# Kernel tuning notes

Measured on AMD Instinct MI355X. Metric: run time of the kernel, lower is better.

## Reference

```python
import jax, jax.numpy as jnp
import numpy as np

B, D, N, L, H, T = 256, 768, 256, 2, 8, 20
HD = D // H

def _ln(x, g, b):
    m = x.mean(-1, keepdims=True)
    v = ((x - m) ** 2).mean(-1, keepdims=True)
    return (x - m) / jnp.sqrt(v + 1e-5) * g + b

def setup_inputs() -> dict:
    key = jax.random.key(0)
    ks = jax.random.split(key, 8)
    kk = jax.random.split(ks[7], 10)
    def w(k, shape):
        return jax.random.normal(k, shape, jnp.float32) * 0.02
    return {
        'feats': jax.random.normal(ks[0], (B, D, N), jnp.float32),
        'past': jax.random.normal(ks[1], (B, 16, 6), jnp.float32),
        'w_qinit': w(ks[2], (121, D)), 'b_qinit': jnp.zeros((D,), jnp.float32),
        'pos_enc': w(ks[3], (1, N, D)),
        'w_pp': w(ks[4], (2, D)), 'b_pp': jnp.zeros((D,), jnp.float32),
        'g_pp': jnp.ones((D,), jnp.float32), 'be_pp': jnp.zeros((D,), jnp.float32),
        'time_emb': w(ks[5], (T, D)),
        'Wq': w(kk[0], (L, D, D)), 'bq': jnp.zeros((L, D), jnp.float32),
        'Wk': w(kk[1], (L, D, D)), 'bk': jnp.zeros((L, D), jnp.float32),
        'Wv': w(kk[2], (L, D, D)), 'bv': jnp.zeros((L, D), jnp.float32),
        'Wo': w(kk[3], (L, D, D)), 'bo': jnp.zeros((L, D), jnp.float32),
        'ln1_g': jnp.ones((L, D), jnp.float32), 'ln1_b': jnp.zeros((L, D), jnp.float32),
        'W1': w(kk[4], (L, D, 4 * D)), 'b1': jnp.zeros((L, 4 * D), jnp.float32),
        'W2': w(kk[5], (L, 4 * D, D)), 'b2': jnp.zeros((L, D), jnp.float32),
        'ln2_g': jnp.ones((L, D), jnp.float32), 'ln2_b': jnp.zeros((L, D), jnp.float32),
        'w_dec1': w(kk[6], (D, D)), 'b_dec1': jnp.zeros((D,), jnp.float32),
        'w_dec2': w(kk[7], (D, 2)), 'b_dec2': jnp.zeros((2,), jnp.float32),
        'intent': jax.random.randint(ks[6], (B,), 0, 3),
    }

def reference(feats, past, w_qinit, b_qinit, pos_enc, w_pp, b_pp, g_pp, be_pp,
              time_emb, Wq, bq, Wk, bk, Wv, bv, Wo, bo, ln1_g, ln1_b,
              W1, b1, W2, b2, ln2_g, ln2_b, w_dec1, b_dec1, w_dec2, b_dec2, intent):
    # tokens: [B, N, D]
    tokens = jnp.transpose(feats, (0, 2, 1)) + pos_enc
    onehot = jax.nn.one_hot(jnp.clip(intent - 1, 0, 2), 3, dtype=tokens.dtype)
    past_flat = past.reshape(B, -1)
    pad = jnp.zeros((B, 22), tokens.dtype)
    context = jnp.concatenate([onehot, past_flat, pad], axis=1) @ w_qinit + b_qinit  # [B, D]
    # precompute cross-attention K/V once per layer (tokens are constant across steps)
    Kh = (jnp.einsum('bnd,lde->lbne', tokens, Wk) + bk[:, None, None, :]).reshape(L, B, N, H, HD)
    Vh = (jnp.einsum('bnd,lde->lbne', tokens, Wv) + bv[:, None, None, :]).reshape(L, B, N, H, HD)
    scale = 1.0 / np.sqrt(HD)

    def step(carry, te):
        ctx, cp = carry
        pq = jax.nn.relu(_ln(cp @ w_pp + b_pp, g_pp, be_pp))
        x = (ctx + pq + te)[:, None, :]  # [B, 1, D]
        for l in range(L):
            q = (_ln(x, ln1_g[l], ln1_b[l]) @ Wq[l] + bq[l]).reshape(B, 1, H, HD)
            s = jnp.einsum('bqhd,bnhd->bhqn', q, Kh[l]) * scale
            a = jax.nn.softmax(s, axis=-1)
            o = jnp.einsum('bhqn,bnhd->bqhd', a, Vh[l]).reshape(B, 1, D) @ Wo[l] + bo[l]
            x = x + o
            h = jax.nn.gelu(_ln(x, ln2_g[l], ln2_b[l]) @ W1[l] + b1[l], approximate=False) @ W2[l] + b2[l]
            x = x + h
        ctx = x[:, 0]
        delta = jax.nn.gelu(ctx @ w_dec1 + b_dec1, approximate=False) @ w_dec2 + b_dec2
        cp = cp + delta
        return (ctx, cp), cp

    init = (context, past[:, -1, 0:2])
    _, ys = jax.lax.scan(step, init, time_emb)  # ys: [T, B, 2]
    return jnp.transpose(ys, (1, 0, 2))
```

## Files before the change

kernel.cpp:

```cpp
#include <hip/hip_runtime.h>
#include <hip/hip_bf16.h>
#include <math.h>

#define B_ 256
#define D_ 768
#define N_ 256
#define L_ 2
#define H_ 8
#define T_ 20
#define HD_ 96
#define D4_ 3072

typedef float f32x4v __attribute__((ext_vector_type(4)));
typedef __bf16 bf16x8v __attribute__((ext_vector_type(8)));

union V16 { uint4 u; bf16x8v v; };

__device__ __forceinline__ ushort f2b(float f) {
    union { float f; unsigned u; } x{f};
    unsigned r = x.u + 0x7fffu + ((x.u >> 16) & 1u);
    return (ushort)(r >> 16);
}
__device__ __forceinline__ float b2f(ushort s) {
    union { unsigned u; float f; } x{(unsigned)s << 16};
    return x.f;
}
__device__ __forceinline__ float gelu_f(float v) {
    return 0.5f * v * (1.0f + erff(v * 0.7071067811865476f));
}
__device__ __forceinline__ float dot8(const float* __restrict__ xp, uint4 u) {
    return xp[0] * b2f((ushort)(u.x & 0xffffu)) + xp[1] * b2f((ushort)(u.x >> 16))
         + xp[2] * b2f((ushort)(u.y & 0xffffu)) + xp[3] * b2f((ushort)(u.y >> 16))
         + xp[4] * b2f((ushort)(u.z & 0xffffu)) + xp[5] * b2f((ushort)(u.z >> 16))
         + xp[6] * b2f((ushort)(u.w & 0xffffu)) + xp[7] * b2f((ushort)(u.w >> 16));
}
__device__ __forceinline__ float blockSum(float v, float* red, int tid) {
    for (int off = 32; off; off >>= 1) v += __shfl_down(v, off, 64);
    int w = tid >> 6, lane = tid & 63;
    if (lane == 0) red[w] = v;
    __syncthreads();
    float r = red[0] + red[1] + red[2] + red[3];
    __syncthreads();
    return r;
}

__global__ __launch_bounds__(256) void context_kernel(const float* __restrict__ past,
                                                      const float* __restrict__ w_qinit,
                                                      const float* __restrict__ b_qinit,
                                                      const int* __restrict__ intent,
                                                      const float* __restrict__ w_pp,
                                                      const float* __restrict__ b_pp,
                                                      const float* __restrict__ g_pp,
                                                      const float* __restrict__ be_pp,
                                                      const float* __restrict__ te0,
                                                      float* __restrict__ x,
                                                      float* __restrict__ cp) {
    int b = blockIdx.x, tid = threadIdx.x;
    __shared__ float ps[96];
    __shared__ int oidx;
    __shared__ float red[4];
    if (tid < 96) ps[tid] = past[b * 96 + tid];
    if (tid == 0) {
        int iv = intent[b] - 1;
        oidx = iv < 0 ? 0 : (iv > 2 ? 2 : iv);
    }
    __syncthreads();
    float ctx[3];
    #pragma unroll
    for (int r = 0; r < 3; ++r) {
        int d = tid + r * 256;
        float acc = w_qinit[oidx * D_ + d] + b_qinit[d];
        #pragma unroll 8
        for (int p = 0; p < 96; ++p) acc += ps[p] * w_qinit[(3 + p) * D_ + d];
        ctx[r] = acc;
    }
    float c0 = ps[90], c1 = ps[91];
    if (tid == 0) { cp[b * 2] = c0; cp[b * 2 + 1] = c1; }
    float t[3];
    float s = 0, ss = 0;
    #pragma unroll
    for (int r = 0; r < 3; ++r) {
        int d = tid + r * 256;
        t[r] = c0 * w_pp[d] + c1 * w_pp[D_ + d] + b_pp[d];
        s += t[r]; ss += t[r] * t[r];
    }
    s = blockSum(s, red, tid);
    ss = blockSum(ss, red, tid);
    float mean = s * (1.0f / D_);
    float var = ss * (1.0f / D_) - mean * mean;
    float rinv = rsqrtf(var + 1e-5f);
    #pragma unroll
    for (int r = 0; r < 3; ++r) {
        int d = tid + r * 256;
        float pq = fmaxf((t[r] - mean) * rinv * g_pp[d] + be_pp[d], 0.0f);
        x[b * D_ + d] = ctx[r] + pq + te0[d];
    }
}

__global__ __launch_bounds__(256) void token_prep(const float* __restrict__ feats,
                                                  const float* __restrict__ pos_enc,
                                                  ushort* __restrict__ tokens) {
    int b = blockIdx.z;
    int d0 = blockIdx.x * 64, n0 = blockIdx.y * 64;
    __shared__ float tile[64][65];
    int tid = threadIdx.x;
    int nl = tid & 63, dl0 = tid >> 6;
    const float* fb = feats + ((size_t)b * D_ + d0) * N_ + n0;
    #pragma unroll
    for (int i = 0; i < 16; ++i) {
        int dl = dl0 + i * 4;
        tile[dl][nl] = fb[(size_t)dl * N_ + nl];
    }
    __syncthreads();
    int dq = (tid & 15) * 4;
    int ng = tid >> 4;
    #pragma unroll
    for (int i = 0; i < 4; ++i) {
        int nl2 = ng + i * 16;
        int n = n0 + nl2;
        float4 p = *(const float4*)(pos_enc + (size_t)n * D_ + d0 + dq);
        ushort4 o;
        o.x = f2b(tile[dq + 0][nl2] + p.x);
        o.y = f2b(tile[dq + 1][nl2] + p.y);
        o.z = f2b(tile[dq + 2][nl2] + p.z);
        o.w = f2b(tile[dq + 3][nl2] + p.w);
        *(ushort4*)&tokens[((size_t)b * N_ + n) * D_ + d0 + dq] = o;
    }
}

__global__ __launch_bounds__(256) void transpose_w(const float* __restrict__ W,
                                                   ushort* __restrict__ out,
                                                   const float* __restrict__ scale,
                                                   int K, int N) {
    __shared__ float t[32][33];
    int k0 = blockIdx.y * 32, n0 = blockIdx.x * 32;
    int tx = threadIdx.x & 31, ty = threadIdx.x >> 5;
    #pragma unroll
    for (int i = 0; i < 4; ++i)
        t[ty + i * 8][tx] = W[(size_t)(k0 + ty + i * 8) * N + n0 + tx];
    __syncthreads();
    #pragma unroll
    for (int i = 0; i < 4; ++i) {
        int n = n0 + ty + i * 8, k = k0 + tx;
        float v = t[tx][ty + i * 8];
        if (scale) v *= scale[k];
        out[(size_t)n * K + k] = f2b(v);
    }
}

__global__ __launch_bounds__(256) void bias_eff_kernel(const float* __restrict__ W,
                                                       const float* __restrict__ bias,
                                                       const float* __restrict__ lb,
                                                       float* __restrict__ be, int Nc) {
    int n = blockIdx.x * 256 + threadIdx.x;
    float a = bias[n];
    for (int k = 0; k < D_; ++k) a += lb[k] * W[(size_t)k * Nc + n];
    be[n] = a;
}

__global__ void kvbias_prep(const float* __restrict__ bk, const float* __restrict__ bv,
                            float* __restrict__ bc) {
    int i = blockIdx.x * 256 + threadIdx.x;
    int mi = i / D_, c = i % D_;
    int l = mi >> 1;
    bc[i] = (mi & 1 ? bv : bk)[l * D_ + c];
}

__global__ __launch_bounds__(256) void kv_gemm_mfma(const ushort* __restrict__ tokens,
                                                    const ushort* __restrict__ Wkvt,
                                                    const float* __restrict__ bias_kv,
                                                    ushort* __restrict__ Kt,
                                                    ushort* __restrict__ Vt) {
    int e0 = blockIdx.x * 128;
    int mi = e0 / D_;
    int ein = e0 % D_;
    int l = mi >> 1, isV = mi & 1;
    int m0 = blockIdx.y * 128;
    int b = m0 >> 8, ntok0 = m0 & 255;
    __shared__ ushort smem[17408];
    ushort* As = smem;
    ushort* Bs = smem + 128 * 40;
    int tid = threadIdx.x;
    int w = tid >> 6, lane = tid & 63, quad = lane >> 4, l16 = lane & 15;
    int wr = w >> 1, wc = w & 1;
    f32x4v acc[4][4];
    #pragma unroll
    for (int i = 0; i < 4; ++i)
        #pragma unroll
        for (int j = 0; j < 4; ++j) acc[i][j] = (f32x4v)(0.0f);

    for (int k0 = 0; k0 < D_; k0 += 32) {
        #pragma unroll
        for (int vv = 0; vv < 2; ++vv) {
            int v = tid + vv * 256;
            int row = v >> 2, kv = v & 3;
            *(uint4*)&As[row * 40 + kv * 8] =
                *(const uint4*)&tokens[(size_t)(m0 + row) * D_ + k0 + kv * 8];
            *(uint4*)&Bs[row * 40 + kv * 8] =
                *(const uint4*)&Wkvt[(size_t)(e0 + row) * D_ + k0 + kv * 8];
        }
        __syncthreads();
        V16 a[4], bb[4];
        #pragma unroll
        for (int i = 0; i < 4; ++i)
            a[i].u = *(const uint4*)&As[(wr * 64 + i * 16 + l16) * 40 + quad * 8];
        #pragma unroll
        for (int j = 0; j < 4; ++j)
            bb[j].u = *(const uint4*)&Bs[(wc * 64 + j * 16 + l16) * 40 + quad * 8];
        #pragma unroll
        for (int i = 0; i < 4; ++i)
            #pragma unroll
            for (int j = 0; j < 4; ++j)
                acc[i][j] = __builtin_amdgcn_mfma_f32_16x16x32_bf16(a[i].v, bb[j].v, acc[i][j], 0, 0, 0);
        __syncthreads();
    }

    float bcol[4];
    #pragma unroll
    for (int j = 0; j < 4; ++j)
        bcol[j] = bias_kv[e0 + wc * 64 + j * 16 + l16];

    ushort* Ct = smem;
    ushort* outbuf = isV ? Vt : Kt;
    #pragma unroll
    for (int i = 0; i < 4; ++i)
        #pragma unroll
        for (int j = 0; j < 4; ++j) {
            int e_l = wc * 64 + j * 16 + l16;
            int m_b = wr * 64 + i * 16 + quad * 4;
            ushort4 p;
            p.x = f2b(acc[i][j][0] + bcol[j]);
            p.y = f2b(acc[i][j][1] + bcol[j]);
            p.z = f2b(acc[i][j][2] + bcol[j]);
            p.w = f2b(acc[i][j][3] + bcol[j]);
            *(ushort4*)&Ct[e_l * 136 + m_b] = p;
        }
    __syncthreads();
    int e_l = tid >> 1, half = tid & 1;
    int c = ein + e_l;
    int h = c / HD_, hd = c % HD_;
    size_t dst = ((((size_t)l * B_ + b) * H_ + h) * HD_ + hd) * N_ + ntok0 + half * 64;
    #pragma unroll
    for (int p8 = 0; p8 < 8; ++p8)
        *(uint4*)&outbuf[dst + p8 * 8] = *(const uint4*)&Ct[e_l * 136 + half * 64 + p8 * 8];
}

template<int AVAR, int OMODE, int STATS, int KSPLIT>
__global__ __launch_bounds__(256) void gemm_s(const void* __restrict__ Av,
                                              const ushort* __restrict__ Bt,
                                              const float* __restrict__ bias,
                                              void* __restrict__ Cv,
                                              int K, int Nc) {
    __shared__ ushort As[64 * 40];
    __shared__ ushort Bs[64 * 40];
    __shared__ float smst[64][2];
    int tid = threadIdx.x;
    int m0 = blockIdx.y * 64, e0 = blockIdx.x * 64;
    int kslice = K / KSPLIT;
    int kbeg = blockIdx.z * kslice, kend = kbeg + kslice;
    int w = tid >> 6, lane = tid & 63, quad = lane >> 4, l16 = lane & 15;

    if (STATS) {
        int row = tid >> 2, part = tid & 3;
        const float* xr = (const float*)Av + (size_t)(m0 + row) * K + part * 192;
        float s = 0, ss = 0;
        #pragma unroll 4
        for (int i = 0; i < 192; i += 4) {
            float4 f = *(const float4*)(xr + i);
            s += f.x + f.y + f.z + f.w;
            ss += f.x * f.x + f.y * f.y + f.z * f.z + f.w * f.w;
        }
        s += __shfl_xor(s, 1, 64);  s += __shfl_xor(s, 2, 64);
        ss += __shfl_xor(ss, 1, 64); ss += __shfl_xor(ss, 2, 64);
        if (part == 0) {
            float mean = s * (1.0f / 768.0f);
            float var = ss * (1.0f / 768.0f) - mean * mean;
            smst[row][0] = mean;
            smst[row][1] = rsqrtf(var + 1e-5f);
        }
        __syncthreads();
    }

    bool doA = tid < 128;
    int t2 = tid & 127;
    f32x4v acc[4];
    #pragma unroll
    for (int i = 0; i < 4; ++i) acc[i] = (f32x4v)(0.0f);

    auto fetch = [&](int kk, int vv) -> uint4 {
        int v = t2 + vv * 128;
        int row = v >> 2, kq = v & 3;
        if (doA) {
            if (AVAR == 0) {
                return *(const uint4*)((const ushort*)Av + (size_t)(m0 + row) * K + kk + kq * 8);
            } else {
                const float* Af = (const float*)Av + (size_t)(m0 + row) * K + kk + kq * 8;
                float4 f0 = *(const float4*)Af;
                float4 f1 = *(const float4*)(Af + 4);
                float mn = smst[row][0], rs = smst[row][1];
                f0.x = (f0.x - mn) * rs; f0.y = (f0.y - mn) * rs;
                f0.z = (f0.z - mn) * rs; f0.w = (f0.w - mn) * rs;
                f1.x = (f1.x - mn) * rs; f1.y = (f1.y - mn) * rs;
                f1.z = (f1.z - mn) * rs; f1.w = (f1.w - mn) * rs;
                uint4 u;
                u.x = (unsigned)f2b(f0.x) | ((unsigned)f2b(f0.y) << 16);
                u.y = (unsigned)f2b(f0.z) | ((unsigned)f2b(f0.w) << 16);
                u.z = (unsigned)f2b(f1.x) | ((unsigned)f2b(f1.y) << 16);
                u.w = (unsigned)f2b(f1.z) | ((unsigned)f2b(f1.w) << 16);
                return u;
            }
        } else {
            return *(const uint4*)&Bt[(size_t)(e0 + row) * K + kk + kq * 8];
        }
    };
    auto stash = [&](int vv, uint4 u) {
        int v = t2 + vv * 128;
        int row = v >> 2, kq = v & 3;
        ushort* dst = doA ? As : Bs;
        *(uint4*)&dst[row * 40 + kq * 8] = u;
    };
    auto compute = [&]() {
        V16 bb;
        bb.u = *(const uint4*)&Bs[(w * 16 + l16) * 40 + quad * 8];
        #pragma unroll
        for (int i = 0; i < 4; ++i) {
            V16 a;
            a.u = *(const uint4*)&As[(i * 16 + l16) * 40 + quad * 8];
            acc[i] = __builtin_amdgcn_mfma_f32_16x16x32_bf16(a.v, bb.v, acc[i], 0, 0, 0);
        }
    };

    {
        uint4 p0 = fetch(kbeg, 0), p1 = fetch(kbeg, 1);
        stash(0, p0); stash(1, p1);
    }
    __syncthreads();
    for (int kk = kbeg + 32; kk < kend; kk += 32) {
        uint4 p0 = fetch(kk, 0), p1 = fetch(kk, 1);
        compute();
        __syncthreads();
        stash(0, p0); stash(1, p1);
        __syncthreads();
    }
    compute();

    int n = e0 + w * 16 + l16;
    float bn = 0.0f;
    if (OMODE != 2 || blockIdx.z == 0) bn = bias[n];
    #pragma unroll
    for (int i = 0; i < 4; ++i) {
        #pragma unroll
        for (int r = 0; r < 4; ++r) {
            int m = m0 + i * 16 + quad * 4 + r;
            float v = acc[i][r] + bn;
            if (OMODE == 1) v = gelu_f(v);
            if (OMODE == 2) atomicAdd((float*)Cv + (size_t)m * Nc + n, v);
            else            ((ushort*)Cv)[(size_t)m * Nc + n] = f2b(v);
        }
    }
}

__global__ __launch_bounds__(256) void attn_fused(const float* __restrict__ x,
                                                  const ushort* __restrict__ Wqt,
                                                  const float* __restrict__ bqe,
                                                  const ushort* __restrict__ Kt,
                                                  const ushort* __restrict__ Vt,
                                                  ushort* __restrict__ att) {
    int b = blockIdx.y, h = blockIdx.x, tid = threadIdx.x;
    __shared__ float xs[768];
    __shared__ float red[4];
    __shared__ float qs[96];
    __shared__ float spart[4][256];
    __shared__ float sc[256];
    __shared__ float opo[96];

    if (tid < 192) *(float4*)&xs[tid * 4] = *(const float4*)&x[(size_t)b * D_ + tid * 4];
    __syncthreads();

    float s = 0, ss = 0;
    #pragma unroll
    for (int r = 0; r < 3; ++r) { float v = xs[tid + r * 256]; s += v; ss += v * v; }
    s = blockSum(s, red, tid);
    ss = blockSum(ss, red, tid);
    float mean = s * (1.0f / D_);
    float var = ss * (1.0f / D_) - mean * mean;
    float rinv = rsqrtf(var + 1e-5f);
    #pragma unroll
    for (int r = 0; r < 3; ++r) { int d = tid + r * 256; xs[d] = (xs[d] - mean) * rinv; }
    __syncthreads();

    if (tid < 192) {
        int j = tid >> 1, kh = tid & 1;
        const ushort* wr = Wqt + (size_t)(h * HD_ + j) * D_ + kh * 384;
        const float* xp = xs + kh * 384;
        float acc = 0.0f;
        #pragma unroll 4
        for (int k = 0; k < 384; k += 8)
            acc += dot8(xp + k, *(const uint4*)&wr[k]);
        acc += __shfl_xor(acc, 1, 64);
        if (kh == 0) qs[j] = (acc + bqe[h * HD_ + j]) * 0.10206207261596575f;
    }
    __syncthreads();

    {
        int hq = tid >> 6, tg = tid & 63;
        const ushort* Kp = Kt + (size_t)(b * H_ + h) * HD_ * N_;
        float s0 = 0, s1 = 0, s2 = 0, s3 = 0;
        #pragma unroll 6
        for (int i = 0; i < 24; ++i) {
            int hd = hq * 24 + i;
            uint2 kk = *(const uint2*)&Kp[hd * N_ + tg * 4];
            float qv = qs[hd];
            s0 += qv * b2f((ushort)(kk.x & 0xffffu));
            s1 += qv * b2f((ushort)(kk.x >> 16));
            s2 += qv * b2f((ushort)(kk.y & 0xffffu));
            s3 += qv * b2f((ushort)(kk.y >> 16));
        }
        float4 sv4;
        sv4.x = s0; sv4.y = s1; sv4.z = s2; sv4.w = s3;
        *(float4*)&spart[hq][tg * 4] = sv4;
    }
    __syncthreads();

    float sv = spart[0][tid] + spart[1][tid] + spart[2][tid] + spart[3][tid];
    int w = tid >> 6, lane = tid & 63;
    float m = sv;
    for (int off = 32; off; off >>= 1) m = fmaxf(m, __shfl_xor(m, off, 64));
    if (lane == 0) red[w] = m;
    __syncthreads();
    m = fmaxf(fmaxf(red[0], red[1]), fmaxf(red[2], red[3]));
    __syncthreads();
    float e = expf(sv - m);
    float tot = blockSum(e, red, tid);
    sc[tid] = e / tot;
    __syncthreads();

    if (tid < 192) {
        int hd = tid >> 1, nh = tid & 1;
        const ushort* Vr = Vt + (size_t)(b * H_ + h) * HD_ * N_ + hd * N_ + nh * 128;
        const float* scp = sc + nh * 128;
        float o = 0.0f;
        #pragma unroll 4
        for (int i = 0; i < 16; ++i)
            o += dot8(scp + i * 8, *(const uint4*)&Vr[i * 8]);
        o += __shfl_xor(o, 1, 64);
        if (nh == 0) opo[hd] = o;
    }
    __syncthreads();
    if (tid < 96) att[(size_t)b * D_ + h * HD_ + tid] = f2b(opo[tid]);
}

__global__ __launch_bounds__(256) void tail_kernel(float* __restrict__ x,
                                                   const ushort* __restrict__ dec1t,
                                                   const float* __restrict__ b_dec1,
                                                   const float* __restrict__ w_dec2,
                                                   const float* __restrict__ b_dec2,
                                                   float* __restrict__ cp,
                                                   float* __restrict__ out,
                                                   const float* __restrict__ time_emb,
                                                   const float* __restrict__ w_pp,
                                                   const float* __restrict__ b_pp,
                                                   const float* __restrict__ g_pp,
                                                   const float* __restrict__ be_pp,
                                                   int t) {
    int b = blockIdx.x, tid = threadIdx.x;
    __shared__ float xs[768];
    __shared__ float red[4];
    #pragma unroll
    for (int r = 0; r < 3; ++r) xs[tid + r * 256] = x[b * D_ + tid + r * 256];
    __syncthreads();
    float d0 = 0, d1 = 0, d2 = 0;
    const ushort* w0 = dec1t + (size_t)tid * D_;
    const ushort* w1 = w0 + (size_t)256 * D_;
    const ushort* w2 = w0 + (size_t)512 * D_;
    #pragma unroll 2
    for (int k = 0; k < 768; k += 8) {
        d0 += dot8(xs + k, *(const uint4*)&w0[k]);
        d1 += dot8(xs + k, *(const uint4*)&w1[k]);
        d2 += dot8(xs + k, *(const uint4*)&w2[k]);
    }
    float v0 = gelu_f(d0 + b_dec1[tid]);
    float v1 = gelu_f(d1 + b_dec1[tid + 256]);
    float v2 = gelu_f(d2 + b_dec1[tid + 512]);
    float p0 = v0 * w_dec2[tid * 2]     + v1 * w_dec2[(tid + 256) * 2]     + v2 * w_dec2[(tid + 512) * 2];
    float p1 = v0 * w_dec2[tid * 2 + 1] + v1 * w_dec2[(tid + 256) * 2 + 1] + v2 * w_dec2[(tid + 512) * 2 + 1];
    p0 = blockSum(p0, red, tid);
    p1 = blockSum(p1, red, tid);
    float c0 = cp[b * 2] + p0 + b_dec2[0];
    float c1 = cp[b * 2 + 1] + p1 + b_dec2[1];
    if (tid == 0) {
        cp[b * 2] = c0;
        cp[b * 2 + 1] = c1;
        out[(b * T_ + t) * 2] = c0;
        out[(b * T_ + t) * 2 + 1] = c1;
    }
    if (t < T_ - 1) {
        const float* te = time_emb + (size_t)(t + 1) * D_;
        float tv[3];
        float s = 0, ss = 0;
        #pragma unroll
        for (int r = 0; r < 3; ++r) {
            int d = tid + r * 256;
            tv[r] = c0 * w_pp[d] + c1 * w_pp[D_ + d] + b_pp[d];
            s += tv[r]; ss += tv[r] * tv[r];
        }
        s = blockSum(s, red, tid);
        ss = blockSum(ss, red, tid);
        float mean = s * (1.0f / D_);
        float var = ss * (1.0f / D_) - mean * mean;
        float rinv = rsqrtf(var + 1e-5f);
        #pragma unroll
        for (int r = 0; r < 3; ++r) {
            int d = tid + r * 256;
            float pq = fmaxf((tv[r] - mean) * rinv * g_pp[d] + be_pp[d], 0.0f);
            x[b * D_ + d] += pq + te[d];
        }
    }
}

extern "C" void kernel_launch(void* const* d_in, const int* in_sizes, int n_in,
                              void* d_out, int out_size, void* d_ws, size_t ws_size,
                              hipStream_t stream) {
    const float* feats   = (const float*)d_in[0];
    const float* past    = (const float*)d_in[1];
    const float* w_qinit = (const float*)d_in[2];
    const float* b_qinit = (const float*)d_in[3];
    const float* pos_enc = (const float*)d_in[4];
    const float* w_pp    = (const float*)d_in[5];
    const float* b_pp    = (const float*)d_in[6];
    const float* g_pp    = (const float*)d_in[7];
    const float* be_pp   = (const float*)d_in[8];
    const float* time_emb= (const float*)d_in[9];
    const float* Wq      = (const float*)d_in[10];
    const float* bq      = (const float*)d_in[11];
    const float* Wk      = (const float*)d_in[12];
    const float* bk      = (const float*)d_in[13];
    const float* Wv      = (const float*)d_in[14];
    const float* bv      = (const float*)d_in[15];
    const float* Wo      = (const float*)d_in[16];
    const float* bo      = (const float*)d_in[17];
    const float* ln1_g   = (const float*)d_in[18];
    const float* ln1_b   = (const float*)d_in[19];
    const float* W1      = (const float*)d_in[20];
    const float* b1      = (const float*)d_in[21];
    const float* W2      = (const float*)d_in[22];
    const float* b2      = (const float*)d_in[23];
    const float* ln2_g   = (const float*)d_in[24];
    const float* ln2_b   = (const float*)d_in[25];
    const float* w_dec1  = (const float*)d_in[26];
    const float* b_dec1  = (const float*)d_in[27];
    const float* w_dec2  = (const float*)d_in[28];
    const float* b_dec2  = (const float*)d_in[29];
    const int*   intent  = (const int*)d_in[30];
    float* out = (float*)d_out;

    const size_t WD = (size_t)D_ * D_;
    const size_t WD4 = (size_t)D_ * D4_;
    const size_t kv_elems = (size_t)L_ * B_ * H_ * HD_ * N_;
    const size_t kv_l = (size_t)B_ * H_ * HD_ * N_;

    char* wp = (char*)d_ws;
    ushort* Kt     = (ushort*)wp; wp += kv_elems * 2;
    ushort* Vt     = (ushort*)wp; wp += kv_elems * 2;
    ushort* tokens = (ushort*)wp; wp += (size_t)B_ * N_ * D_ * 2;
    ushort* Wkvt   = (ushort*)wp; wp += 4 * WD * 2;
    ushort* Wqt    = (ushort*)wp; wp += 2 * WD * 2;
    ushort* Wot    = (ushort*)wp; wp += 2 * WD * 2;
    ushort* W1t    = (ushort*)wp; wp += 2 * WD4 * 2;
    ushort* W2t    = (ushort*)wp; wp += 2 * WD4 * 2;
    ushort* dec1t  = (ushort*)wp; wp += WD * 2;
    float* bias_kv = (float*)wp;  wp += 4 * D_ * 4;
    float* bqe     = (float*)wp;  wp += 2 * D_ * 4;
    float* b1e     = (float*)wp;  wp += 2 * D4_ * 4;
    float* x       = (float*)wp;  wp += (size_t)B_ * D_ * 4;
    ushort* attbuf = (ushort*)wp; wp += (size_t)B_ * D_ * 2;
    ushort* h1     = (ushort*)wp; wp += (size_t)B_ * D4_ * 2;
    float* cp      = (float*)wp;  wp += (size_t)B_ * 2 * 4;

    context_kernel<<<B_, 256, 0, stream>>>(past, w_qinit, b_qinit, intent,
                                           w_pp, b_pp, g_pp, be_pp, time_emb, x, cp);
    token_prep<<<dim3(12, 4, 256), 256, 0, stream>>>(feats, pos_enc, tokens);
    kvbias_prep<<<12, 256, 0, stream>>>(bk, bv, bias_kv);
    for (int l = 0; l < L_; ++l) {
        transpose_w<<<dim3(24, 24), 256, 0, stream>>>(Wk + l * WD, Wkvt + (2 * l + 0) * WD, nullptr, D_, D_);
        transpose_w<<<dim3(24, 24), 256, 0, stream>>>(Wv + l * WD, Wkvt + (2 * l + 1) * WD, nullptr, D_, D_);
        transpose_w<<<dim3(24, 24), 256, 0, stream>>>(Wq + l * WD, Wqt + l * WD, ln1_g + l * D_, D_, D_);
        transpose_w<<<dim3(24, 24), 256, 0, stream>>>(Wo + l * WD, Wot + l * WD, nullptr, D_, D_);
        transpose_w<<<dim3(96, 24), 256, 0, stream>>>(W1 + l * WD4, W1t + l * WD4, ln2_g + l * D_, D_, D4_);
        transpose_w<<<dim3(24, 96), 256, 0, stream>>>(W2 + l * WD4, W2t + l * WD4, nullptr, D4_, D_);
        bias_eff_kernel<<<3, 256, 0, stream>>>(Wq + l * WD, bq + l * D_, ln1_b + l * D_, bqe + l * D_, D_);
        bias_eff_kernel<<<12, 256, 0, stream>>>(W1 + l * WD4, b1 + l * D4_, ln2_b + l * D_, b1e + l * D4_, D4_);
    }
    transpose_w<<<dim3(24, 24), 256, 0, stream>>>(w_dec1, dec1t, nullptr, D_, D_);

    kv_gemm_mfma<<<dim3(24, 512), 256, 0, stream>>>(tokens, Wkvt, bias_kv, Kt, Vt);

    for (int t = 0; t < T_; ++t) {
        for (int l = 0; l < L_; ++l) {
            attn_fused<<<dim3(H_, B_), 256, 0, stream>>>(x, Wqt + l * WD, bqe + l * D_,
                                                         Kt + l * kv_l, Vt + l * kv_l, attbuf);
            gemm_s<0, 2, 0, 4><<<dim3(12, 4, 4), 256, 0, stream>>>(attbuf, Wot + l * WD,
                                                                   bo + l * D_, x, D_, D_);
            gemm_s<1, 1, 1, 1><<<dim3(48, 4), 256, 0, stream>>>(x, W1t + l * WD4,
                                                                b1e + l * D4_, h1, D_, D4_);
            gemm_s<0, 2, 0, 4><<<dim3(12, 4, 4), 256, 0, stream>>>(h1, W2t + l * WD4,
                                                                   b2 + l * D_, x, D4_, D_);
        }
        tail_kernel<<<B_, 256, 0, stream>>>(x, dec1t, b_dec1, w_dec2, b_dec2, cp, out,
                                            time_emb, w_pp, b_pp, g_pp, be_pp, t);
    }
}
```

Measured before the change: 7.202 ms.

## Double-buffer GEMM tiles via direct global-to-LDS loads and widen attention K reads

The KV projection GEMM and the generic gemm_s kernel now stage their tiles with global_load_lds straight into double-buffered shared memory, so the next K-slice loads while MFMAs run on the current one. This removes the register round trip and one barrier per iteration. The padded row stride of 40 becomes an unpadded 32, which may add LDS bank conflicts on the MFMA operand reads. Attention score computation now reads K with 16-byte loads and combines half-waves with a shuffle.

Measured after the change: 6.781 ms. -5.8%, faster.

```diff
diff --git a/kernel.cpp b/kernel.cpp
--- a/kernel.cpp
+++ b/kernel.cpp
@@ -42,6 +42,11 @@
     float r = red[0] + red[1] + red[2] + red[3];
     __syncthreads();
     return r;
+}
+__device__ __forceinline__ void gl_lds16(const ushort* g, ushort* l) {
+    __builtin_amdgcn_global_load_lds((const __attribute__((address_space(1))) unsigned int*)g,
+                                     (__attribute__((address_space(3))) unsigned int*)l,
+                                     16, 0, 0);
 }
 
 __global__ __launch_bounds__(256) void context_kernel(const float* __restrict__ past,
@@ -177,9 +182,7 @@
     int l = mi >> 1, isV = mi & 1;
     int m0 = blockIdx.y * 128;
     int b = m0 >> 8, ntok0 = m0 & 255;
-    __shared__ ushort smem[17408];
-    ushort* As = smem;
-    ushort* Bs = smem + 128 * 40;
+    __shared__ __align__(16) ushort smem[17408];
     int tid = threadIdx.x;
     int w = tid >> 6, lane = tid & 63, quad = lane >> 4, l16 = lane & 15;
     int wr = w >> 1, wc = w & 1;
@@ -189,30 +192,41 @@
         #pragma unroll
         for (int j = 0; j < 4; ++j) acc[i][j] = (f32x4v)(0.0f);
 
-    for (int k0 = 0; k0 < D_; k0 += 32) {
+    auto stage = [&](int buf, int k0) {
+        ushort* Ab = smem + buf * 8192;
+        ushort* Bb = Ab + 4096;
         #pragma unroll
         for (int vv = 0; vv < 2; ++vv) {
             int v = tid + vv * 256;
-            int row = v >> 2, kv = v & 3;
-            *(uint4*)&As[row * 40 + kv * 8] =
-                *(const uint4*)&tokens[(size_t)(m0 + row) * D_ + k0 + kv * 8];
-            *(uint4*)&Bs[row * 40 + kv * 8] =
-                *(const uint4*)&Wkvt[(size_t)(e0 + row) * D_ + k0 + kv * 8];
-        }
-        __syncthreads();
+            int row = v >> 2, kq = v & 3;
+            gl_lds16(&tokens[(size_t)(m0 + row) * D_ + k0 + kq * 8], Ab + w * 512 + vv * 2048);
+            gl_lds16(&Wkvt[(size_t)(e0 + row) * D_ + k0 + kq * 8],   Bb + w * 512 + vv * 2048);
+        }
+    };
+
+    stage(0, 0);
+    asm volatile("s_waitcnt vmcnt(0)" ::: "memory");
+    __syncthreads();
+    int cur = 0;
+    for (int k0 = 0; k0 < D_; k0 += 32) {
+        if (k0 + 32 < D_) stage(cur ^ 1, k0 + 32);
+        const ushort* Ab = smem + cur * 8192;
+        const ushort* Bb = Ab + 4096;
         V16 a[4], bb[4];
         #pragma unroll
         for (int i = 0; i < 4; ++i)
-            a[i].u = *(const uint4*)&As[(wr * 64 + i * 16 + l16) * 40 + quad * 8];
+            a[i].u = *(const uint4*)&Ab[(wr * 64 + i * 16 + l16) * 32 + quad * 8];
         #pragma unroll
         for (int j = 0; j < 4; ++j)
-            bb[j].u = *(const uint4*)&Bs[(wc * 64 + j * 16 + l16) * 40 + quad * 8];
+            bb[j].u = *(const uint4*)&Bb[(wc * 64 + j * 16 + l16) * 32 + quad * 8];
         #pragma unroll
         for (int i = 0; i < 4; ++i)
             #pragma unroll
             for (int j = 0; j < 4; ++j)
                 acc[i][j] = __builtin_amdgcn_mfma_f32_16x16x32_bf16(a[i].v, bb[j].v, acc[i][j], 0, 0, 0);
+        asm volatile("s_waitcnt vmcnt(0)" ::: "memory");
         __syncthreads();
+        cur ^= 1;
     }
 
     float bcol[4];
@@ -251,8 +265,8 @@
                                               const float* __restrict__ bias,
                                               void* __restrict__ Cv,
                                               int K, int Nc) {
-    __shared__ ushort As[64 * 40];
-    __shared__ ushort Bs[64 * 40];
+    __shared__ __align__(16) ushort As[2][2048];
+    __shared__ __align__(16) ushort Bs[2][2048];
     __shared__ float smst[64][2];
     int tid = threadIdx.x;
     int m0 = blockIdx.y * 64, e0 = blockIdx.x * 64;
@@ -281,68 +295,93 @@
         __syncthreads();
     }
 
-    bool doA = tid < 128;
+    bool doA = w < 2;
     int t2 = tid & 127;
     f32x4v acc[4];
     #pragma unroll
     for (int i = 0; i < 4; ++i) acc[i] = (f32x4v)(0.0f);
 
-    auto fetch = [&](int kk, int vv) -> uint4 {
+    auto fetchA1 = [&](int kk, int vv) -> uint4 {
         int v = t2 + vv * 128;
         int row = v >> 2, kq = v & 3;
-        if (doA) {
-            if (AVAR == 0) {
-                return *(const uint4*)((const ushort*)Av + (size_t)(m0 + row) * K + kk + kq * 8);
-            } else {
-                const float* Af = (const float*)Av + (size_t)(m0 + row) * K + kk + kq * 8;
-                float4 f0 = *(const float4*)Af;
-                float4 f1 = *(const float4*)(Af + 4);
-                float mn = smst[row][0], rs = smst[row][1];
-                f0.x = (f0.x - mn) * rs; f0.y = (f0.y - mn) * rs;
-                f0.z = (f0.z - mn) * rs; f0.w = (f0.w - mn) * rs;
-                f1.x = (f1.x - mn) * rs; f1.y = (f1.y - mn) * rs;
-                f1.z = (f1.z - mn) * rs; f1.w = (f1.w - mn) * rs;
-                uint4 u;
-                u.x = (unsigned)f2b(f0.x) | ((unsigned)f2b(f0.y) << 16);
-                u.y = (unsigned)f2b(f0.z) | ((unsigned)f2b(f0.w) << 16);
-                u.z = (unsigned)f2b(f1.x) | ((unsigned)f2b(f1.y) << 16);
-                u.w = (unsigned)f2b(f1.z) | ((unsigned)f2b(f1.w) << 16);
-                return u;
-            }
-        } else {
-            return *(const uint4*)&Bt[(size_t)(e0 + row) * K + kk + kq * 8];
-        }
+        const float* Af = (const float*)Av + (size_t)(m0 + row) * K + kk + kq * 8;
+        float4 f0 = *(const float4*)Af;
+        float4 f1 = *(const float4*)(Af + 4);
+        float mn = smst[row][0], rs = smst[row][1];
+        f0.x = (f0.x - mn) * rs; f0.y = (f0.y - mn) * rs;
+        f0.z = (f0.z - mn) * rs; f0.w = (f0.w - mn) * rs;
+        f1.x = (f1.x - mn) * rs; f1.y = (f1.y - mn) * rs;
+        f1.z = (f1.z - mn) * rs; f1.w = (f1.w - mn) * rs;
+        uint4 u;
+        u.x = (unsigned)f2b(f0.x) | ((unsigned)f2b(f0.y) << 16);
+        u.y = (unsigned)f2b(f0.z) | ((unsigned)f2b(f0.w) << 16);
+        u.z = (unsigned)f2b(f1.x) | ((unsigned)f2b(f1.y) << 16);
+        u.w = (unsigned)f2b(f1.z) | ((unsigned)f2b(f1.w) << 16);
+        return u;
     };
-    auto stash = [&](int vv, uint4 u) {
+    auto stashA = [&](int buf, int vv, uint4 u) {
         int v = t2 + vv * 128;
         int row = v >> 2, kq = v & 3;
-        ushort* dst = doA ? As : Bs;
-        *(uint4*)&dst[row * 40 + kq * 8] = u;
+        *(uint4*)&As[buf][row * 32 + kq * 8] = u;
     };
-    auto compute = [&]() {
+    auto stageA0 = [&](int buf, int kk) {
+        #pragma unroll
+        for (int vv = 0; vv < 2; ++vv) {
+            int v = t2 + vv * 128;
+            int row = v >> 2, kq = v & 3;
+            gl_lds16((const ushort*)Av + (size_t)(m0 + row) * K + kk + kq * 8,
+                     &As[buf][w * 512 + vv * 1024]);
+        }
+    };
+    auto stageB = [&](int buf, int kk) {
+        int wb = w - 2;
+        #pragma unroll
+        for (int vv = 0; vv < 2; ++vv) {
+            int v = t2 + vv * 128;
+            int row = v >> 2, kq = v & 3;
+            gl_lds16(&Bt[(size_t)(e0 + row) * K + kk + kq * 8],
+                     &Bs[buf][wb * 512 + vv * 1024]);
+        }
+    };
+    auto compute = [&](int buf) {
         V16 bb;
-        bb.u = *(const uint4*)&Bs[(w * 16 + l16) * 40 + quad * 8];
+        bb.u = *(const uint4*)&Bs[buf][(w * 16 + l16) * 32 + quad * 8];
         #pragma unroll
         for (int i = 0; i < 4; ++i) {
             V16 a;
-            a.u = *(const uint4*)&As[(i * 16 + l16) * 40 + quad * 8];
+            a.u = *(const uint4*)&As[buf][(i * 16 + l16) * 32 + quad * 8];
             acc[i] = __builtin_amdgcn_mfma_f32_16x16x32_bf16(a.v, bb.v, acc[i], 0, 0, 0);
         }
     };
 
-    {
-        uint4 p0 = fetch(kbeg, 0), p1 = fetch(kbeg, 1);
-        stash(0, p0); stash(1, p1);
-    }
-    __syncthreads();
+    if (doA) {
+        if (AVAR == 0) {
+            stageA0(0, kbeg);
+        } else {
+            uint4 p0 = fetchA1(kbeg, 0), p1 = fetchA1(kbeg, 1);
+            stashA(0, 0, p0); stashA(0, 1, p1);
+        }
+    } else {
+        stageB(0, kbeg);
+    }
+    asm volatile("s_waitcnt vmcnt(0)" ::: "memory");
+    __syncthreads();
+    int cur = 0;
     for (int kk = kbeg + 32; kk < kend; kk += 32) {
-        uint4 p0 = fetch(kk, 0), p1 = fetch(kk, 1);
-        compute();
+        uint4 p0, p1;
+        if (doA) {
+            if (AVAR == 0) stageA0(cur ^ 1, kk);
+            else { p0 = fetchA1(kk, 0); p1 = fetchA1(kk, 1); }
+        } else {
+            stageB(cur ^ 1, kk);
+        }
+        compute(cur);
+        if (AVAR == 1 && doA) { stashA(cur ^ 1, 0, p0); stashA(cur ^ 1, 1, p1); }
+        asm volatile("s_waitcnt vmcnt(0)" ::: "memory");
         __syncthreads();
-        stash(0, p0); stash(1, p1);
-        __syncthreads();
-    }
-    compute();
+        cur ^= 1;
+    }
+    compute(cur);
 
     int n = e0 + w * 16 + l16;
     float bn = 0.0f;
@@ -367,6 +406,7 @@
                                                   const ushort* __restrict__ Vt,
                                                   ushort* __restrict__ att) {
     int b = blockIdx.y, h = blockIdx.x, tid = threadIdx.x;
+    int w = tid >> 6, lane = tid & 63;
     __shared__ float xs[768];
     __shared__ float red[4];
     __shared__ float qs[96];
@@ -403,27 +443,38 @@
     __syncthreads();
 
     {
-        int hq = tid >> 6, tg = tid & 63;
+        int r2 = lane >> 5, tg = lane & 31;
         const ushort* Kp = Kt + (size_t)(b * H_ + h) * HD_ * N_;
-        float s0 = 0, s1 = 0, s2 = 0, s3 = 0;
-        #pragma unroll 6
-        for (int i = 0; i < 24; ++i) {
-            int hd = hq * 24 + i;
-            uint2 kk = *(const uint2*)&Kp[hd * N_ + tg * 4];
+        float s8[8];
+        #pragma unroll
+        for (int j = 0; j < 8; ++j) s8[j] = 0.0f;
+        #pragma unroll 4
+        for (int i = 0; i < 12; ++i) {
+            int hd = w * 24 + i * 2 + r2;
+            uint4 kk = *(const uint4*)&Kp[hd * N_ + tg * 8];
             float qv = qs[hd];
-            s0 += qv * b2f((ushort)(kk.x & 0xffffu));
-            s1 += qv * b2f((ushort)(kk.x >> 16));
-            s2 += qv * b2f((ushort)(kk.y & 0xffffu));
-            s3 += qv * b2f((ushort)(kk.y >> 16));
-        }
-        float4 sv4;
-        sv4.x = s0; sv4.y = s1; sv4.z = s2; sv4.w = s3;
-        *(float4*)&spart[hq][tg * 4] = sv4;
+            s8[0] += qv * b2f((ushort)(kk.x & 0xffffu));
+            s8[1] += qv * b2f((ushort)(kk.x >> 16));
+            s8[2] += qv * b2f((ushort)(kk.y & 0xffffu));
+            s8[3] += qv * b2f((ushort)(kk.y >> 16));
+            s8[4] += qv * b2f((ushort)(kk.z & 0xffffu));
+            s8[5] += qv * b2f((ushort)(kk.z >> 16));
+            s8[6] += qv * b2f((ushort)(kk.w & 0xffffu));
+            s8[7] += qv * b2f((ushort)(kk.w >> 16));
+        }
+        #pragma unroll
+        for (int j = 0; j < 8; ++j) s8[j] += __shfl_xor(s8[j], 32, 64);
+        if (r2 == 0) {
+            float4 lo, hi;
+            lo.x = s8[0]; lo.y = s8[1]; lo.z = s8[2]; lo.w = s8[3];
+            hi.x = s8[4]; hi.y = s8[5]; hi.z = s8[6]; hi.w = s8[7];
+            *(float4*)&spart[w][tg * 8] = lo;
+            *(float4*)&spart[w][tg * 8 + 4] = hi;
+        }
     }
     __syncthreads();
 
     float sv = spart[0][tid] + spart[1][tid] + spart[2][tid] + spart[3][tid];
-    int w = tid >> 6, lane = tid & 63;
     float m = sv;
     for (int off = 32; off; off >>= 1) m = fmaxf(m, __shfl_xor(m, off, 64));
     if (lane == 0) red[w] = m;
```
